# Kernel tuning notes

Hardware: AMD Instinct MI355X
Metric: run time of the kernel (lower is better)

The kernel has to match this reference:

```python
import jax, jax.numpy as jnp
import numpy as np


def _rgb_to_hue(x):
    # x: [B, 3, H, W] in [0,1]; returns hue channel [B, H, W] in [0,1),
    # matching skimage.color.rgb2hsv's hue definition.
    r, g, b = x[:, 0], x[:, 1], x[:, 2]
    maxc = jnp.max(x, axis=1)
    minc = jnp.min(x, axis=1)
    delta = maxc - minc
    safe = jnp.where(delta == 0, 1.0, delta)  # avoid div-by-zero
    h = jnp.where(
        maxc == r, (g - b) / safe,
        jnp.where(maxc == g, 2.0 + (b - r) / safe, 4.0 + (r - g) / safe),
    )
    h = jnp.where(delta == 0, 0.0, (h / 6.0) % 1.0)
    return h


def setup_inputs() -> dict:
    key = jax.random.key(0)
    k1, k2 = jax.random.split(key)
    B, C, H, W = 32, 3, 512, 512
    predict = jax.random.uniform(k1, (B, C, H, W), dtype=jnp.float32)
    target = jax.random.uniform(k2, (B, C, H, W), dtype=jnp.float32)
    return {"predict": predict, "target": target}


def reference(predict, target):
    hp = _rgb_to_hue(predict)  # [B, H, W]
    ht = _rgb_to_hue(target)
    diff = jnp.abs(hp - ht)
    mask = (diff > 0.5).astype(diff.dtype)
    mask_ = (diff < 0.5).astype(diff.dtype)
    # mean(|diff*mask_|) + mean(|diff*mask - 0.5*mask|); first term already >= 0
    loss = jnp.mean(diff * mask_) + jnp.mean(jnp.abs((diff - 0.5) * mask))
    return loss
```

## Files before the change

### kernel.cpp

```cpp
#include <hip/hip_runtime.h>

#define HW_PLANE (512 * 512)
#define NPIX     (32 * HW_PLANE)
#define NBLOCKS  2048
#define KSTEP (8 * 3 * HW_PLANE)

__device__ __forceinline__ float hue1(float r, float g, float b) {
    float maxc  = fmaxf(r, fmaxf(g, b));
    float minc  = fminf(r, fminf(g, b));
    float delta = maxc - minc;
    float safe  = (delta == 0.0f) ? 1.0f : delta;
    float rs    = __builtin_amdgcn_rcpf(safe);
    float hr = (g - b) * rs;
    float hg = 2.0f + (b - r) * rs;
    float hb = 4.0f + (r - g) * rs;
    float h  = (maxc == r) ? hr : ((maxc == g) ? hg : hb);
    h = h * (1.0f / 6.0f);
    h = h - floorf(h);
    return (delta == 0.0f) ? 0.0f : h;
}

__device__ __forceinline__ void acc_diff(float hp, float ht, float& lo, float& hi) {
    float d = fabsf(hp - ht);
    if (d < 0.5f)      lo += d;
    else if (d > 0.5f) hi += d - 0.5f;
}

__global__ void __launch_bounds__(256)
hsv_partial(const float* __restrict__ pred, const float* __restrict__ targ,
            float2* __restrict__ partial) {
    const int tid  = blockIdx.x * 256 + threadIdx.x;
    const int p    = tid << 2;
    const int bimg = p >> 18;
    const int pix  = p & (HW_PLANE - 1);
    const int base = bimg * (3 * HW_PLANE) + pix;

    float4 P[4][3], T[4][3];
    #pragma unroll
    for (int k = 0; k < 4; ++k) {
        const float* pp = pred + base + k * KSTEP;
        const float* tt = targ + base + k * KSTEP;
        P[k][0] = *(const float4*)(pp);
        P[k][1] = *(const float4*)(pp + HW_PLANE);
        P[k][2] = *(const float4*)(pp + 2 * HW_PLANE);
        T[k][0] = *(const float4*)(tt);
        T[k][1] = *(const float4*)(tt + HW_PLANE);
        T[k][2] = *(const float4*)(tt + 2 * HW_PLANE);
    }

    float lo = 0.0f, hi = 0.0f;
    #pragma unroll
    for (int k = 0; k < 4; ++k) {
        float4 pr = P[k][0], pg = P[k][1], pb = P[k][2];
        float4 tr = T[k][0], tg = T[k][1], tb = T[k][2];
        acc_diff(hue1(pr.x, pg.x, pb.x), hue1(tr.x, tg.x, tb.x), lo, hi);
        acc_diff(hue1(pr.y, pg.y, pb.y), hue1(tr.y, tg.y, tb.y), lo, hi);
        acc_diff(hue1(pr.z, pg.z, pb.z), hue1(tr.z, tg.z, tb.z), lo, hi);
        acc_diff(hue1(pr.w, pg.w, pb.w), hue1(tr.w, tg.w, tb.w), lo, hi);
    }

    for (int off = 32; off > 0; off >>= 1) {
        lo += __shfl_down(lo, off, 64);
        hi += __shfl_down(hi, off, 64);
    }
    __shared__ float slo[4], shi[4];
    int lane = threadIdx.x & 63;
    int wave = threadIdx.x >> 6;
    if (lane == 0) { slo[wave] = lo; shi[wave] = hi; }
    __syncthreads();
    if (threadIdx.x == 0) {
        partial[blockIdx.x] =
            make_float2(slo[0] + slo[1] + slo[2] + slo[3],
                        shi[0] + shi[1] + shi[2] + shi[3]);
    }
}

__global__ void __launch_bounds__(256)
hsv_final(const float2* __restrict__ partial, float* __restrict__ out, int nblocks) {
    float lo = 0.0f, hi = 0.0f;
    for (int i = threadIdx.x; i < nblocks; i += blockDim.x) {
        float2 p = partial[i];
        lo += p.x; hi += p.y;
    }
    for (int off = 32; off > 0; off >>= 1) {
        lo += __shfl_down(lo, off, 64);
        hi += __shfl_down(hi, off, 64);
    }
    __shared__ float slo[4], shi[4];
    int lane = threadIdx.x & 63;
    int wave = threadIdx.x >> 6;
    if (lane == 0) { slo[wave] = lo; shi[wave] = hi; }
    __syncthreads();
    if (threadIdx.x == 0) {
        float L = slo[0] + slo[1] + slo[2] + slo[3];
        float H = shi[0] + shi[1] + shi[2] + shi[3];
        out[0] = (L + H) * (1.0f / (float)NPIX);
    }
}

extern "C" void kernel_launch(void* const* d_in, const int* in_sizes, int n_in,
                              void* d_out, int out_size, void* d_ws, size_t ws_size,
                              hipStream_t stream) {
    const float* pred = (const float*)d_in[0];
    const float* targ = (const float*)d_in[1];
    float*  out     = (float*)d_out;
    float2* partial = (float2*)d_ws;

    hsv_partial<<<NBLOCKS, 256, 0, stream>>>(pred, targ, partial);
    hsv_final<<<1, 256, 0, stream>>>(partial, out, NBLOCKS);
}
```

Measured before the change: 218.2 us.

## Give each thread 16 contiguous pixels with nontemporal loads

```diff
diff --git a/kernel.cpp b/kernel.cpp
--- a/kernel.cpp
+++ b/kernel.cpp
@@ -3,7 +3,12 @@
 #define HW_PLANE (512 * 512)
 #define NPIX     (32 * HW_PLANE)
 #define NBLOCKS  2048
-#define KSTEP (8 * 3 * HW_PLANE)
+
+typedef float vfloat4 __attribute__((ext_vector_type(4)));
+
+__device__ __forceinline__ vfloat4 ldnt(const float* p) {
+    return __builtin_nontemporal_load((const vfloat4*)p);
+}
 
 __device__ __forceinline__ float hue1(float r, float g, float b) {
     float maxc  = fmaxf(r, fmaxf(g, b));
@@ -26,33 +31,32 @@
     else if (d > 0.5f) hi += d - 0.5f;
 }
 
-__global__ void __launch_bounds__(256)
+__global__ void __launch_bounds__(256, 2)
 hsv_partial(const float* __restrict__ pred, const float* __restrict__ targ,
             float2* __restrict__ partial) {
     const int tid  = blockIdx.x * 256 + threadIdx.x;
-    const int p    = tid << 2;
-    const int bimg = p >> 18;
+    const int p    = tid << 4;
+    const int img  = p >> 18;
     const int pix  = p & (HW_PLANE - 1);
-    const int base = bimg * (3 * HW_PLANE) + pix;
+    const int base = img * (3 * HW_PLANE) + pix;
+    const float* pp = pred + base;
+    const float* tt = targ + base;
 
-    float4 P[4][3], T[4][3];
+    vfloat4 P[3][4], T[3][4];
     #pragma unroll
-    for (int k = 0; k < 4; ++k) {
-        const float* pp = pred + base + k * KSTEP;
-        const float* tt = targ + base + k * KSTEP;
-        P[k][0] = *(const float4*)(pp);
-        P[k][1] = *(const float4*)(pp + HW_PLANE);
-        P[k][2] = *(const float4*)(pp + 2 * HW_PLANE);
-        T[k][0] = *(const float4*)(tt);
-        T[k][1] = *(const float4*)(tt + HW_PLANE);
-        T[k][2] = *(const float4*)(tt + 2 * HW_PLANE);
+    for (int c = 0; c < 3; ++c) {
+        #pragma unroll
+        for (int k = 0; k < 4; ++k) {
+            P[c][k] = ldnt(pp + c * HW_PLANE + 4 * k);
+            T[c][k] = ldnt(tt + c * HW_PLANE + 4 * k);
+        }
     }
 
     float lo = 0.0f, hi = 0.0f;
     #pragma unroll
     for (int k = 0; k < 4; ++k) {
-        float4 pr = P[k][0], pg = P[k][1], pb = P[k][2];
-        float4 tr = T[k][0], tg = T[k][1], tb = T[k][2];
+        vfloat4 pr = P[0][k], pg = P[1][k], pb = P[2][k];
+        vfloat4 tr = T[0][k], tg = T[1][k], tb = T[2][k];
         acc_diff(hue1(pr.x, pg.x, pb.x), hue1(tr.x, tg.x, tb.x), lo, hi);
         acc_diff(hue1(pr.y, pg.y, pb.y), hue1(tr.y, tg.y, tb.y), lo, hi);
         acc_diff(hue1(pr.z, pg.z, pb.z), hue1(tr.z, tg.z, tb.z), lo, hi);
```

New measurement: 232.9 us. 1.07x slower.
